# Kernel optimization log

Measured on AMD Instinct MI355X. Metric: run time of the kernel, lower is better.

Reference implementation:

```python
import jax, jax.numpy as jnp
import numpy as np

D = 8192          # Hadamard dimension (power of 2)
K = 1024          # number of selected columns = len(idx)
NORMALIZED = True
SCALE = np.float32(1.0 / np.sqrt(D))


def setup_inputs() -> dict:
    key = jax.random.key(0)
    k1, k2 = jax.random.split(key)
    u = jax.random.normal(k1, (4, 2048, K), dtype=jnp.float32)
    idx = jnp.sort(jax.random.randint(k2, (K,), 0, D, dtype=jnp.int32))
    return {"u": u, "idx": idx}


def _fwht(x):
    """Unnormalized fast Walsh-Hadamard transform over last dim. x: (B, D)."""
    B, d = x.shape
    h = 1
    while h < d:  # log2(D) static iterations -> jit-friendly
        y = x.reshape(B, d // (2 * h), 2, h)
        a, b = y[:, :, 0, :], y[:, :, 1, :]
        x = jnp.stack([a + b, a - b], axis=2).reshape(B, d)
        h *= 2
    return x


def reference(u, idx):
    # x = H_D[:, idx] @ u  (optionally / sqrt(D))
    # = FWHT(scatter(u at idx into zeros(D))) since H @ e_j = H[:, j]
    orig = u.shape[:-1]
    u2 = u.reshape(-1, u.shape[-1])                      # (B, K)
    z = jnp.zeros((u2.shape[0], D), u.dtype).at[:, idx].add(u2)  # (B, D)
    out = _fwht(z)
    if NORMALIZED:
        out = out * SCALE
    return out.reshape(*orig, D)
```

## Files before the change

### kernel.cpp

```cpp
#include <hip/hip_runtime.h>

#define D      8192
#define K      1024
#define BLOCK  256
#define GRID_MAX 2048
#define SCALE  0.011048543456039806f

typedef float nat_f4 __attribute__((ext_vector_type(4)));

__device__ __forceinline__ int swz4(int f) { return f ^ ((f >> 3) & 7); }

__device__ __forceinline__ void fwht32(float* x) {
#pragma unroll
    for (int s = 0; s < 5; ++s) {
        const int h = 1 << s;
#pragma unroll
        for (int g = 0; g < 32; g += 2 * h)
#pragma unroll
            for (int e = 0; e < h; ++e) {
                float a = x[g + e], b = x[g + e + h];
                x[g + e]     = a + b;
                x[g + e + h] = a - b;
            }
    }
}

__device__ __forceinline__ void fwht8(float* x) {
#pragma unroll
    for (int s = 0; s < 3; ++s) {
        const int h = 1 << s;
#pragma unroll
        for (int g = 0; g < 8; g += 2 * h)
#pragma unroll
            for (int e = 0; e < h; ++e) {
                float a = x[g + e], b = x[g + e + h];
                x[g + e]     = a + b;
                x[g + e + h] = a - b;
            }
    }
}

__global__ __launch_bounds__(BLOCK, 5)
void UpProjectFastHadamardTransform_80101140070867_kernel(
    const float* __restrict__ u, const int* __restrict__ idx,
    float* __restrict__ out, int nrows)
{
    __shared__ float4 lds4[D / 4];
    float* lds = (float*)lds4;
    const int t = threadIdx.x;

    const int4 id = ((const int4*)idx)[t];
    const int c  = t & 7;
    const int wb = 4 * ((t >> 2) ^ ((t >> 5) & 7)) + (t & 3);

    int r = blockIdx.x;
    float4 v = ((const float4*)(u + (size_t)r * K))[t];

    for (; r < nrows; ) {
        __syncthreads();

#pragma unroll
        for (int j = 0; j < D / 4 / BLOCK; ++j)
            lds4[t + j * BLOCK] = make_float4(0.f, 0.f, 0.f, 0.f);
        __syncthreads();

        {
            int f, a;
            f = id.x >> 2; a = 4 * swz4(f) + (id.x & 3); atomicAdd(&lds[a], v.x);
            f = id.y >> 2; a = 4 * swz4(f) + (id.y & 3); atomicAdd(&lds[a], v.y);
            f = id.z >> 2; a = 4 * swz4(f) + (id.z & 3); atomicAdd(&lds[a], v.z);
            f = id.w >> 2; a = 4 * swz4(f) + (id.w & 3); atomicAdd(&lds[a], v.w);
        }

        const int rn = r + (int)gridDim.x;
        if (rn < nrows) v = ((const float4*)(u + (size_t)rn * K))[t];
        __syncthreads();

        float x[32];

#pragma unroll
        for (int g = 0; g < 8; ++g) {
            float4 a = lds4[t * 8 + (g ^ c)];
            x[4*g+0] = a.x; x[4*g+1] = a.y; x[4*g+2] = a.z; x[4*g+3] = a.w;
        }
        fwht32(x);
        __syncthreads();
#pragma unroll
        for (int j = 0; j < 32; ++j) lds[j * 256 + wb] = x[j];
        __syncthreads();

#pragma unroll
        for (int g = 0; g < 8; ++g) {
            float4 a = lds4[t * 8 + (g ^ c)];
            x[4*g+0] = a.x; x[4*g+1] = a.y; x[4*g+2] = a.z; x[4*g+3] = a.w;
        }
        fwht32(x);
        __syncthreads();
#pragma unroll
        for (int j = 0; j < 32; ++j) lds[j * 256 + wb] = x[j];
        __syncthreads();

#pragma unroll
        for (int g = 0; g < 8; ++g) {
            float4 a = lds4[t * 8 + (g ^ c)];
            x[4*g+0] = a.x; x[4*g+1] = a.y; x[4*g+2] = a.z; x[4*g+3] = a.w;
        }
#pragma unroll
        for (int g2 = 0; g2 < 4; ++g2) fwht8(&x[g2 * 8]);

        float* orow = out + (size_t)r * D + ((t >> 3) * 32 + (t & 7) * 4);
#pragma unroll
        for (int e = 0; e < 8; ++e) {
            nat_f4 o = { x[e] * SCALE, x[8 + e] * SCALE,
                         x[16 + e] * SCALE, x[24 + e] * SCALE };
            __builtin_nontemporal_store(o, (nat_f4*)(orow + e * 1024));
        }

        r = rn;
    }
}

extern "C" void kernel_launch(void* const* d_in, const int* in_sizes, int n_in,
                              void* d_out, int out_size, void* d_ws, size_t ws_size,
                              hipStream_t stream) {
    const float* u   = (const float*)d_in[0];
    const int*   idx = (const int*)d_in[1];
    float*       out = (float*)d_out;
    const int rows = in_sizes[0] / K;
    const int grid = rows < GRID_MAX ? rows : GRID_MAX;
    hipLaunchKernelGGL(UpProjectFastHadamardTransform_80101140070867_kernel,
                       dim3(grid), dim3(BLOCK), 0, stream, u, idx, out, rows);
}
```

Baseline: 305.0 us.

## Partition FWHT so each wavefront owns a 2048-slice, removing block barriers

Each of the four wavefronts now owns a contiguous 2048-element slice of the row. It scatters only the indices that fall in its range, located by a wave-wide count over idx, then runs the first two radix-32 stages on its own slice without block-level barriers. Only the final cross-slice radix-8 stage needs one __syncthreads, which cuts the per-row barrier count from about six to two. In exchange the u loads become scalar and gathered per element, the registers per thread grow, and load balance depends on how idx is distributed, with a fallback loop for slices holding more than 512 indices.

```diff
diff --git a/kernel.cpp b/kernel.cpp
--- a/kernel.cpp
+++ b/kernel.cpp
@@ -5,10 +5,10 @@
 #define BLOCK  256
 #define GRID_MAX 2048
 #define SCALE  0.011048543456039806f
+#define MAXE   8
 
 typedef float nat_f4 __attribute__((ext_vector_type(4)));
 
-__device__ __forceinline__ int swz4(int f) { return f ^ ((f >> 3) & 7); }
 
 __device__ __forceinline__ void fwht32(float* x) {
 #pragma unroll
@@ -47,68 +47,121 @@
 {
     __shared__ float4 lds4[D / 4];
     float* lds = (float*)lds4;
-    const int t = threadIdx.x;
+    const int T = threadIdx.x;
+    const int w = T >> 6;
+    const int l = T & 63;
 
-    const int4 id = ((const int4*)idx)[t];
-    const int c  = t & 7;
-    const int wb = 4 * ((t >> 2) ^ ((t >> 5) & 7)) + (t & 3);
+    int clo = 0, chi = 0;
+    const int rlo = w << 11, rhi = rlo + 2048;
+#pragma unroll
+    for (int s = 0; s < 16; ++s) {
+        const int v = idx[l + 64 * s];
+        clo += (v < rlo);
+        chi += (v < rhi);
+    }
+#pragma unroll
+    for (int d = 32; d; d >>= 1) {
+        clo += __shfl_xor(clo, d, 64);
+        chi += __shfl_xor(chi, d, 64);
+    }
+    const int lo = clo, hi = chi;
+    const int Jw = (hi - lo + 63) >> 6;
+
+    int aj[MAXE];
+#pragma unroll
+    for (int j = 0; j < MAXE; ++j) {
+        const int k = lo + l + (j << 6);
+        int a = -1;
+        if (j < Jw && k < hi) {
+            const int r = idx[k] & 2047;
+            const int f = r >> 2;
+            a = 4 * (f ^ ((f >> 3) & 7)) + (r & 3);
+        }
+        aj[j] = a;
+    }
+
+    const int ldsW   = w << 11;
+    const int lds4W  = w << 9;
+    const int c1     = l & 7;
+    const int c2     = ((l << 1) + (l >> 5)) & 7;
+    const int p1_lo2 = l >> 2, p1_hi = l >> 5, p1_e = l & 3;
+    const int p2r_b4 = ((l & 31) << 4) + ((l >> 5) << 3);
+    const int p2w_b  = ((((l >> 5) | (w << 1)) << 10) |
+                        (((l >> 2) & 7) << 2) | (l & 3));
 
     int r = blockIdx.x;
-    float4 v = ((const float4*)(u + (size_t)r * K))[t];
+    const int stride = (int)gridDim.x;
 
-    for (; r < nrows; ) {
+    float vc[MAXE], vn[MAXE];
+    {
+        const float* ur = u + (size_t)r * K;
+#pragma unroll
+        for (int j = 0; j < MAXE; ++j)
+            vc[j] = (aj[j] >= 0) ? ur[lo + l + (j << 6)] : 0.f;
+    }
+
+    while (r < nrows) {
         __syncthreads();
 
 #pragma unroll
-        for (int j = 0; j < D / 4 / BLOCK; ++j)
-            lds4[t + j * BLOCK] = make_float4(0.f, 0.f, 0.f, 0.f);
-        __syncthreads();
+        for (int q = 0; q < 8; ++q)
+            lds4[lds4W + (q << 6) + l] = make_float4(0.f, 0.f, 0.f, 0.f);
 
-        {
-            int f, a;
-            f = id.x >> 2; a = 4 * swz4(f) + (id.x & 3); atomicAdd(&lds[a], v.x);
-            f = id.y >> 2; a = 4 * swz4(f) + (id.y & 3); atomicAdd(&lds[a], v.y);
-            f = id.z >> 2; a = 4 * swz4(f) + (id.z & 3); atomicAdd(&lds[a], v.z);
-            f = id.w >> 2; a = 4 * swz4(f) + (id.w & 3); atomicAdd(&lds[a], v.w);
+#pragma unroll
+        for (int j = 0; j < MAXE; ++j)
+            if (aj[j] >= 0) atomicAdd(&lds[ldsW + aj[j]], vc[j]);
+        if (Jw > MAXE) {
+            const float* ur = u + (size_t)r * K;
+            for (int k = lo + l + (MAXE << 6); k < hi; k += 64) {
+                const int rr = idx[k] & 2047;
+                const int f  = rr >> 2;
+                atomicAdd(&lds[ldsW + 4 * (f ^ ((f >> 3) & 7)) + (rr & 3)], ur[k]);
+            }
         }
 
-        const int rn = r + (int)gridDim.x;
-        if (rn < nrows) v = ((const float4*)(u + (size_t)rn * K))[t];
-        __syncthreads();
+        const int rn = r + stride;
+        if (rn < nrows) {
+            const float* ur = u + (size_t)rn * K;
+#pragma unroll
+            for (int j = 0; j < MAXE; ++j)
+                vn[j] = (aj[j] >= 0) ? ur[lo + l + (j << 6)] : 0.f;
+        }
 
         float x[32];
 
 #pragma unroll
         for (int g = 0; g < 8; ++g) {
-            float4 a = lds4[t * 8 + (g ^ c)];
+            const float4 a = lds4[lds4W + (l << 3) + (g ^ c1)];
             x[4*g+0] = a.x; x[4*g+1] = a.y; x[4*g+2] = a.z; x[4*g+3] = a.w;
         }
         fwht32(x);
-        __syncthreads();
 #pragma unroll
-        for (int j = 0; j < 32; ++j) lds[j * 256 + wb] = x[j];
+        for (int j = 0; j < 32; ++j) {
+            const int f = (j << 4) + p1_lo2;
+            lds[ldsW + 4 * (f ^ ((2 * j + p1_hi) & 7)) + p1_e] = x[j];
+        }
+
+#pragma unroll
+        for (int g = 0; g < 8; ++g) {
+            const float4 a = lds4[lds4W + p2r_b4 + (g ^ c2)];
+            x[4*g+0] = a.x; x[4*g+1] = a.y; x[4*g+2] = a.z; x[4*g+3] = a.w;
+        }
+        fwht32(x);
+#pragma unroll
+        for (int m = 0; m < 32; ++m)
+            lds[p2w_b + (m << 5)] = x[m];
+
         __syncthreads();
 
 #pragma unroll
-        for (int g = 0; g < 8; ++g) {
-            float4 a = lds4[t * 8 + (g ^ c)];
-            x[4*g+0] = a.x; x[4*g+1] = a.y; x[4*g+2] = a.z; x[4*g+3] = a.w;
-        }
-        fwht32(x);
-        __syncthreads();
-#pragma unroll
-        for (int j = 0; j < 32; ++j) lds[j * 256 + wb] = x[j];
-        __syncthreads();
-
-#pragma unroll
-        for (int g = 0; g < 8; ++g) {
-            float4 a = lds4[t * 8 + (g ^ c)];
-            x[4*g+0] = a.x; x[4*g+1] = a.y; x[4*g+2] = a.z; x[4*g+3] = a.w;
+        for (int h = 0; h < 8; ++h) {
+            const float4 a = lds4[(h << 8) + T];
+            x[h] = a.x; x[8 + h] = a.y; x[16 + h] = a.z; x[24 + h] = a.w;
         }
 #pragma unroll
-        for (int g2 = 0; g2 < 4; ++g2) fwht8(&x[g2 * 8]);
+        for (int q = 0; q < 4; ++q) fwht8(&x[q * 8]);
 
-        float* orow = out + (size_t)r * D + ((t >> 3) * 32 + (t & 7) * 4);
+        float* orow = out + (size_t)r * D + ((T >> 3) * 32 + (T & 7) * 4);
 #pragma unroll
         for (int e = 0; e < 8; ++e) {
             nat_f4 o = { x[e] * SCALE, x[8 + e] * SCALE,
@@ -116,6 +169,8 @@
             __builtin_nontemporal_store(o, (nat_f4*)(orow + e * 1024));
         }
 
+#pragma unroll
+        for (int j = 0; j < MAXE; ++j) vc[j] = vn[j];
         r = rn;
     }
 }
```

New measurement: 396.0 us. 29.8% more time.

## Make middle FWHT pass wave-local to drop block-wide barriers

Applied to the files above, without the earlier changes.

Reorganizes the three-pass FWHT data exchange so that the first transpose and the second 32-point pass stay within each 64-lane wave's own 2048-element slice of LDS. This removes two of the block-wide __syncthreads between passes. The final pass reads the layout in a new order, with new swizzle indices. It relies on implicit wave-level ordering of LDS writes and reads without an explicit barrier, which is a correctness risk if the compiler or hardware reorders them.

```diff
diff --git a/kernel.cpp b/kernel.cpp
--- a/kernel.cpp
+++ b/kernel.cpp
@@ -7,6 +7,7 @@
 #define SCALE  0.011048543456039806f
 
 typedef float nat_f4 __attribute__((ext_vector_type(4)));
+
 
 __device__ __forceinline__ int swz4(int f) { return f ^ ((f >> 3) & 7); }
 
@@ -47,21 +48,31 @@
 {
     __shared__ float4 lds4[D / 4];
     float* lds = (float*)lds4;
-    const int t = threadIdx.x;
+    const int T = threadIdx.x;
+    const int w = T >> 6;
+    const int l = T & 63;
 
-    const int4 id = ((const int4*)idx)[t];
-    const int c  = t & 7;
-    const int wb = 4 * ((t >> 2) ^ ((t >> 5) & 7)) + (t & 3);
+    const int4 id = ((const int4*)idx)[T];
+
+    const int ldsW   = w << 11;
+    const int lds4W  = w << 9;
+    const int c1     = T & 7;
+    const int c2     = ((l << 1) + (l >> 5)) & 7;
+    const int p1_lo2 = l >> 2, p1_hi = l >> 5, p1_e = l & 3;
+    const int p2r_b4 = ((l & 31) << 4) + ((l >> 5) << 3);
+    const int p2w_b  = ((((l >> 5) | (w << 1)) << 10) |
+                        (((l >> 2) & 7) << 2) | (l & 3));
 
     int r = blockIdx.x;
-    float4 v = ((const float4*)(u + (size_t)r * K))[t];
+    const int stride = (int)gridDim.x;
+    float4 v = ((const float4*)(u + (size_t)r * K))[T];
 
-    for (; r < nrows; ) {
+    while (r < nrows) {
         __syncthreads();
 
 #pragma unroll
-        for (int j = 0; j < D / 4 / BLOCK; ++j)
-            lds4[t + j * BLOCK] = make_float4(0.f, 0.f, 0.f, 0.f);
+        for (int q = 0; q < 8; ++q)
+            lds4[(q << 8) + T] = make_float4(0.f, 0.f, 0.f, 0.f);
         __syncthreads();
 
         {
@@ -72,43 +83,45 @@
             f = id.w >> 2; a = 4 * swz4(f) + (id.w & 3); atomicAdd(&lds[a], v.w);
         }
 
-        const int rn = r + (int)gridDim.x;
-        if (rn < nrows) v = ((const float4*)(u + (size_t)rn * K))[t];
+        const int rn = r + stride;
+        if (rn < nrows) v = ((const float4*)(u + (size_t)rn * K))[T];
         __syncthreads();
 
         float x[32];
 
 #pragma unroll
         for (int g = 0; g < 8; ++g) {
-            float4 a = lds4[t * 8 + (g ^ c)];
+            const float4 a = lds4[(T << 3) + (g ^ c1)];
             x[4*g+0] = a.x; x[4*g+1] = a.y; x[4*g+2] = a.z; x[4*g+3] = a.w;
         }
         fwht32(x);
-        __syncthreads();
 #pragma unroll
-        for (int j = 0; j < 32; ++j) lds[j * 256 + wb] = x[j];
+        for (int j = 0; j < 32; ++j) {
+            const int f = (j << 4) + p1_lo2;
+            lds[ldsW + 4 * (f ^ ((2 * j + p1_hi) & 7)) + p1_e] = x[j];
+        }
+
+#pragma unroll
+        for (int g = 0; g < 8; ++g) {
+            const float4 a = lds4[lds4W + p2r_b4 + (g ^ c2)];
+            x[4*g+0] = a.x; x[4*g+1] = a.y; x[4*g+2] = a.z; x[4*g+3] = a.w;
+        }
+        fwht32(x);
+#pragma unroll
+        for (int m = 0; m < 32; ++m)
+            lds[p2w_b + (m << 5)] = x[m];
+
         __syncthreads();
 
 #pragma unroll
-        for (int g = 0; g < 8; ++g) {
-            float4 a = lds4[t * 8 + (g ^ c)];
-            x[4*g+0] = a.x; x[4*g+1] = a.y; x[4*g+2] = a.z; x[4*g+3] = a.w;
-        }
-        fwht32(x);
-        __syncthreads();
-#pragma unroll
-        for (int j = 0; j < 32; ++j) lds[j * 256 + wb] = x[j];
-        __syncthreads();
-
-#pragma unroll
-        for (int g = 0; g < 8; ++g) {
-            float4 a = lds4[t * 8 + (g ^ c)];
-            x[4*g+0] = a.x; x[4*g+1] = a.y; x[4*g+2] = a.z; x[4*g+3] = a.w;
+        for (int h = 0; h < 8; ++h) {
+            const float4 a = lds4[(h << 8) + T];
+            x[h] = a.x; x[8 + h] = a.y; x[16 + h] = a.z; x[24 + h] = a.w;
         }
 #pragma unroll
-        for (int g2 = 0; g2 < 4; ++g2) fwht8(&x[g2 * 8]);
+        for (int q = 0; q < 4; ++q) fwht8(&x[q * 8]);
 
-        float* orow = out + (size_t)r * D + ((t >> 3) * 32 + (t & 7) * 4);
+        float* orow = out + (size_t)r * D + ((T >> 3) * 32 + (T & 7) * 4);
 #pragma unroll
         for (int e = 0; e < 8; ++e) {
             nat_f4 o = { x[e] * SCALE, x[8 + e] * SCALE,
```

Result: slower. 358.3 us (+17.5%).
